# Kernel tuning notes

Hardware: AMD Instinct MI355X
Metric: run time of the kernel (lower is better)

The kernel has to match this reference:

```python
import jax, jax.numpy as jnp
import numpy as np

NEAR, FAR, N_SAMPLES = 1.0, 6.0, 64
FAR_APPEND = 1000.0


def setup_inputs() -> dict:
    key = jax.random.key(0)
    ks = jax.random.split(key, 8)
    B, R = 2, 4096
    # pixel coords in a 128x128 image
    x_pix = jax.random.uniform(ks[0], (B, R, 2), dtype=jnp.float32) * 128.0
    # plausible pinhole intrinsics (fx=fy=128, cx=cy=64)
    K = jnp.array([[128.0, 0.0, 64.0], [0.0, 128.0, 64.0], [0.0, 0.0, 1.0]], dtype=jnp.float32)
    intrinsics = jnp.tile(K[None], (B, 1, 1))
    # identity rotation, small translation cam2world
    c2w = jnp.eye(4, dtype=jnp.float32).at[:3, 3].set(jnp.array([0.1, -0.2, 0.5]))
    cam2world = jnp.tile(c2w[None], (B, 1, 1))
    H = 256
    W1 = jax.random.normal(ks[1], (3, H), dtype=jnp.float32) / np.sqrt(3.0)
    b1 = jnp.zeros((H,), jnp.float32)
    W2 = jax.random.normal(ks[2], (H, H), dtype=jnp.float32) / np.sqrt(H)
    b2 = jnp.zeros((H,), jnp.float32)
    W3 = jax.random.normal(ks[3], (H, 4), dtype=jnp.float32) / np.sqrt(H)
    b3 = jnp.zeros((4,), jnp.float32)
    return {"x_pix": x_pix, "intrinsics": intrinsics, "cam2world": cam2world,
            "W1": W1, "b1": b1, "W2": W2, "b2": b2, "W3": W3, "b3": b3}


def _radiance_field(pts, W1, b1, W2, b2, W3, b3):
    # pts: (B, N, 3) -> sigma (B, N, 1), rad (B, N, 3)
    h = jax.nn.relu(pts @ W1 + b1)
    h = jax.nn.relu(h @ W2 + b2)
    o = h @ W3 + b3
    return jax.nn.relu(o[..., :1]), jax.nn.sigmoid(o[..., 1:])


def _get_world_rays(x_pix, intrinsics, cam2world):
    B, R, _ = x_pix.shape
    inv_K = jnp.linalg.inv(intrinsics)  # (B,3,3)
    xy_hom = jnp.concatenate([x_pix, jnp.ones((B, R, 1), x_pix.dtype)], axis=-1)  # (B,R,3)
    dirs_cam = jnp.einsum("bij,brj->bri", inv_K, xy_hom)  # unnormalized cam-frame dirs
    dirs_hom = jnp.concatenate([dirs_cam, jnp.zeros((B, R, 1), x_pix.dtype)], axis=-1)  # w=0 vector
    dirs_world = jnp.einsum("bij,brj->bri", cam2world, dirs_hom)[..., :3]
    origins = jnp.broadcast_to(cam2world[:, None, :3, 3], (B, R, 3))
    return origins, dirs_world


def _volume_integral(z_vals, sigmas, radiances):
    # z_vals: (S,); sigmas: (B,R,S,1); radiances: (B,R,S,3)
    dists = jnp.diff(z_vals, append=jnp.array([FAR_APPEND], z_vals.dtype))  # (S,)
    alpha = 1.0 - jnp.exp(-sigmas * dists[None, None, :, None])  # (B,R,S,1)
    Ts = jnp.cumprod(1.0 - alpha, axis=2)  # inclusive cumprod, matching torch
    weights = alpha * Ts  # (B,R,S,1)
    rgb = jnp.sum(weights * radiances, axis=2)  # (B,R,3)
    depth_map = jnp.einsum("brsv,s->brv", weights, z_vals)  # (B,R,1)
    return rgb, depth_map, weights


def reference(x_pix, intrinsics, cam2world, W1, b1, W2, b2, W3, b3):
    B, R = x_pix.shape[0], x_pix.shape[1]
    ros, rds = _get_world_rays(x_pix, intrinsics, cam2world)
    z_vals = jnp.linspace(NEAR, FAR, N_SAMPLES, dtype=x_pix.dtype)  # (S,)
    pts = ros[:, :, None, :] + rds[:, :, None, :] * z_vals[None, None, :, None]  # (B,R,S,3)
    pts = pts.reshape(B, -1, 3)
    sigma, rad = _radiance_field(pts, W1, b1, W2, b2, W3, b3)
    sigma = sigma.reshape(B, R, N_SAMPLES, 1)
    rad = rad.reshape(B, R, N_SAMPLES, 3)
    rgb, depth_map, weights = _volume_integral(z_vals, sigma, rad)
    accum = jnp.sum(weights, axis=-2)  # (B,R,1)
    rgb = rgb + (1.0 - accum)  # white background
    return rgb, depth_map
```

## Files before the change

### kernel.cpp

```cpp
#include <hip/hip_runtime.h>

typedef unsigned short u16;
typedef _Float16 f16x8 __attribute__((ext_vector_type(8)));
typedef _Float16 f16x4 __attribute__((ext_vector_type(4)));
typedef float    f32x4 __attribute__((ext_vector_type(4)));

#define NRAYS 8192

#define WS_W2T  0
#define WS_B2   131072
#define WS_W3PT 132096
#define WS_B3   136192
#define WS_W1   136208
#define WS_B1   139280
#define WS_INTR 140304
#define WS_C2W  140384

__device__ __forceinline__ float bf2f(u16 u){
  union { unsigned int i; float f; } v; v.i = ((unsigned int)u) << 16; return v.f;
}
__device__ __forceinline__ u16 f2h(float f){
  union { _Float16 h; u16 u; } v; v.h = (_Float16)f;
  return v.u;
}
__device__ __forceinline__ int detect_bf16(const void* intr){
  return (((const u16*)intr)[0] == 0x4300u) ? 1 : 0;
}

__device__ __forceinline__ void conv_arr(const void* src, float* dst, int n, int bf, int tid){
  if (bf){
    const u16* s = (const u16*)src;
    for (int i = tid; i < n; i += 256) dst[i] = bf2f(s[i]);
  } else {
    const float* s = (const float*)src;
    for (int i = tid; i < n; i += 256) dst[i] = s[i];
  }
}

__global__ void prep(const void* __restrict__ W2, const void* __restrict__ W1,
                     const void* __restrict__ b1, const void* __restrict__ b2,
                     const void* __restrict__ W3, const void* __restrict__ b3,
                     const void* __restrict__ intr, const void* __restrict__ c2w,
                     char* __restrict__ ws)
{
  const int bf = detect_bf16(intr);
  const int t = threadIdx.x;
  if (blockIdx.x == 16){
    conv_arr(W1,  (float*)(ws + WS_W1),  768,  bf, t);
    conv_arr(b1,  (float*)(ws + WS_B1),  256,  bf, t);
    conv_arr(b2,  (float*)(ws + WS_B2),  256,  bf, t);
    conv_arr(b3,  (float*)(ws + WS_B3),  4,    bf, t);
    conv_arr(intr,(float*)(ws + WS_INTR),18,   bf, t);
    conv_arr(c2w, (float*)(ws + WS_C2W), 32,   bf, t);
    {
      u16* w3p = (u16*)(ws + WS_W3PT);
      for (int i = t; i < 1024; i += 256){
        int j = i >> 8, k = i & 255;
        float v = bf ? bf2f(((const u16*)W3)[k*4 + j]) : ((const float*)W3)[k*4 + j];
        w3p[i] = f2h(v);
      }
    }
    return;
  }
  __shared__ u16 tile[64][72];
  const int bx = blockIdx.x & 3;
  const int by = blockIdx.x >> 2;
  const int c = t & 63, rb = t >> 6;
  u16* W2T = (u16*)(ws + WS_W2T);
  #pragma unroll
  for (int rr = 0; rr < 64; rr += 4){
    int k = bx*64 + rr + rb;
    int n = by*64 + c;
    float v = bf ? bf2f(((const u16*)W2)[k*256 + n]) : ((const float*)W2)[k*256 + n];
    tile[rr + rb][c] = f2h(v);
  }
  __syncthreads();
  #pragma unroll
  for (int rr = 0; rr < 64; rr += 4){
    int n = by*64 + rr + rb;
    int k = bx*64 + c;
    W2T[n*256 + k] = tile[c][rr + rb];
  }
}

__global__ __launch_bounds__(256, 2) void nerf_fused(
    const void* __restrict__ x_pix,
    const void* __restrict__ intr,
    const char* __restrict__ ws,
    float* __restrict__ out)
{
  __shared__ __align__(16) u16 h1s[128 * 256];
  __shared__ __align__(16) float obuf[128 * 4];

  const int tid = threadIdx.x;
  const int l   = tid & 63;
  const int w   = tid >> 6;
  const int ray = w >> 1;
  const int rayg = blockIdx.x * 2 + ray;
  const int bb   = rayg >> 12;
  const int bf   = detect_bf16(intr);

  const float* intrf = (const float*)(ws + WS_INTR);
  const float* c2wf  = (const float*)(ws + WS_C2W);
  const float* W1f   = (const float*)(ws + WS_W1);
  const float* b1f   = (const float*)(ws + WS_B1);
  const float* b2f   = (const float*)(ws + WS_B2);
  const u16*   W3pT  = (const u16*)(ws + WS_W3PT);
  const u16*   W2T   = (const u16*)(ws + WS_W2T);

  float px, py;
  if (bf){
    px = bf2f(((const u16*)x_pix)[rayg*2 + 0]);
    py = bf2f(((const u16*)x_pix)[rayg*2 + 1]);
  } else {
    px = ((const float*)x_pix)[rayg*2 + 0];
    py = ((const float*)x_pix)[rayg*2 + 1];
  }
  float Ka[9], Mm[16];
  #pragma unroll
  for (int i = 0; i < 9;  i++) Ka[i] = intrf[bb*9  + i];
  #pragma unroll
  for (int i = 0; i < 16; i++) Mm[i] = c2wf[bb*16 + i];
  float a = Ka[0], b_ = Ka[1], c = Ka[2];
  float d = Ka[3], e  = Ka[4], f = Ka[5];
  float g = Ka[6], h  = Ka[7], i9 = Ka[8];
  float det = a*(e*i9 - f*h) - b_*(d*i9 - f*g) + c*(d*h - e*g);
  float inv = 1.0f / det;
  float i00 = (e*i9 - f*h)*inv, i01 = (c*h - b_*i9)*inv, i02 = (b_*f - c*e)*inv;
  float i10 = (f*g - d*i9)*inv, i11 = (a*i9 - c*g)*inv, i12 = (c*d - a*f)*inv;
  float i20 = (d*h - e*g)*inv,  i21 = (b_*g - a*h)*inv, i22 = (a*e - b_*d)*inv;
  float dcx = i00*px + i01*py + i02;
  float dcy = i10*px + i11*py + i12;
  float dcz = i20*px + i21*py + i22;
  float dx = Mm[0]*dcx + Mm[1]*dcy + Mm[2]*dcz;
  float dy = Mm[4]*dcx + Mm[5]*dcy + Mm[6]*dcz;
  float dz = Mm[8]*dcx + Mm[9]*dcy + Mm[10]*dcz;
  float ox = Mm[3], oy = Mm[7], oz = Mm[11];

  const int kbase = (w & 1)*128 + l*2;
  float aa0, aa1, gg0, gg1;
  {
    float2 r0 = *(const float2*)(W1f + kbase);
    float2 r1 = *(const float2*)(W1f + 256 + kbase);
    float2 r2 = *(const float2*)(W1f + 512 + kbase);
    float2 rb = *(const float2*)(b1f + kbase);
    aa0 = ox*r0.x + oy*r1.x + oz*r2.x + rb.x;
    aa1 = ox*r0.y + oy*r1.y + oz*r2.y + rb.y;
    gg0 = dx*r0.x + dy*r1.x + dz*r2.x;
    gg1 = dx*r0.y + dy*r1.y + dz*r2.y;
  }
  const float step = 5.0f / 63.0f;
  const int chunk_w = ((w & 1) << 4) + (l >> 2);
  const int sub_b   = (l & 3) << 2;
  {
    char* hb = (char*)h1s + (ray*64)*512;
    #pragma unroll 8
    for (int s = 0; s < 64; s++){
      float z = 1.0f + step * (float)s;
      u16 e0 = f2h(fmaxf(fmaf(gg0, z, aa0), 0.0f));
      u16 e1 = f2h(fmaxf(fmaf(gg1, z, aa1), 0.0f));
      unsigned pk = (unsigned)e0 | ((unsigned)e1 << 16);
      *(unsigned*)(hb + s*512 + ((chunk_w ^ (s & 7)) << 4) + sub_b) = pk;
    }
  }
  __syncthreads();

  const int col = l & 15;
  const int q   = l >> 4;
  const int c7  = col & 7;
  const int nbase = w * 64;

  f32x4 acc[4][8];
  #pragma unroll
  for (int nt = 0; nt < 4; nt++)
    #pragma unroll
    for (int mt = 0; mt < 8; mt++)
      acc[nt][mt] = (f32x4){0.f, 0.f, 0.f, 0.f};

  const u16* Ab = W2T + (nbase + col)*256 + q*8;
  const char* hbase = (const char*)h1s;

  f16x8 afc[4], bfc[8];
  #pragma unroll
  for (int nt = 0; nt < 4; nt++)
    afc[nt] = *(const f16x8*)(Ab + nt*16*256);
  {
    const int swz = (q ^ c7) << 4;
    #pragma unroll
    for (int mt = 0; mt < 8; mt++)
      bfc[mt] = *(const f16x8*)(hbase + (mt*16 + col)*512 + swz);
  }

  #pragma unroll
  for (int kc = 0; kc < 8; kc++){
    f16x8 afn[4], bfn[8];
    if (kc < 7){
      #pragma unroll
      for (int nt = 0; nt < 4; nt++)
        afn[nt] = *(const f16x8*)(Ab + nt*16*256 + (kc+1)*32);
      const int swz = (((kc+1)*4 + q) ^ c7) << 4;
      #pragma unroll
      for (int mt = 0; mt < 8; mt++)
        bfn[mt] = *(const f16x8*)(hbase + (mt*16 + col)*512 + swz);
    }
    #pragma unroll
    for (int nt = 0; nt < 4; nt++)
      #pragma unroll
      for (int mt = 0; mt < 8; mt++)
        acc[nt][mt] = __builtin_amdgcn_mfma_f32_16x16x32_f16(
            afc[nt], bfc[mt], acc[nt][mt], 0, 0, 0);
    if (kc < 7){
      #pragma unroll
      for (int nt = 0; nt < 4; nt++) afc[nt] = afn[nt];
      #pragma unroll
      for (int mt = 0; mt < 8; mt++) bfc[mt] = bfn[mt];
    }
  }

  f16x8 w3frag[8];
  {
    const u16* wp = W3pT + (col & 3)*256 + q*8;
    #pragma unroll
    for (int kc = 0; kc < 8; kc++)
      w3frag[kc] = *(const f16x8*)(wp + kc*32);
  }

  __syncthreads();
  #pragma unroll
  for (int nt = 0; nt < 4; nt++){
    const int n2 = nbase + nt*16 + q*4;
    const int chb = n2 >> 3;
    const int sub = (n2 & 7) * 2;
    f32x4 b2v = *(const f32x4*)(b2f + n2);
    #pragma unroll
    for (int mt = 0; mt < 8; mt++){
      const int m = mt*16 + col;
      f32x4 t = acc[nt][mt] + b2v;
      f16x4 hq;
      hq.x = (_Float16)fmaxf(t.x, 0.0f);
      hq.y = (_Float16)fmaxf(t.y, 0.0f);
      hq.z = (_Float16)fmaxf(t.z, 0.0f);
      hq.w = (_Float16)fmaxf(t.w, 0.0f);
      *(f16x4*)((char*)h1s + m*512 + ((chb ^ (m & 7)) << 4) + sub) = hq;
    }
  }
  __syncthreads();

  f32x4 acc3[2];
  acc3[0] = (f32x4){0.f,0.f,0.f,0.f};
  acc3[1] = (f32x4){0.f,0.f,0.f,0.f};
  #pragma unroll
  for (int mt3 = 0; mt3 < 2; mt3++){
    const int mrow = w*32 + mt3*16 + col;
    const int m7 = mrow & 7;
    #pragma unroll
    for (int kc = 0; kc < 8; kc++){
      f16x8 a3 = *(const f16x8*)((const char*)h1s + mrow*512 + (((kc*4 + q) ^ m7) << 4));
      acc3[mt3] = __builtin_amdgcn_mfma_f32_16x16x32_f16(a3, w3frag[kc], acc3[mt3], 0, 0, 0);
    }
  }
  if (col < 4){
    #pragma unroll
    for (int mt3 = 0; mt3 < 2; mt3++)
      #pragma unroll
      for (int rr = 0; rr < 4; rr++)
        obuf[(w*32 + mt3*16 + q*4 + rr)*4 + col] = acc3[mt3][rr];
  }
  __syncthreads();

  if (w < 2){
    const int m = w*64 + l;
    f32x4 oj  = *(const f32x4*)&obuf[m*4];
    f32x4 b3v = *(const f32x4*)(ws + WS_B3);
    float o_s0 = oj.x + b3v.x;
    float o_s1 = oj.y + b3v.y;
    float o_s2 = oj.z + b3v.z;
    float o_s3 = oj.w + b3v.w;

    const float zc    = 1.0f + step * (float)l;
    const float znext = (l == 63) ? 1000.0f : (1.0f + step * (float)(l + 1));
    const float dist  = znext - zc;
    float sigma = fmaxf(o_s0, 0.0f);
    float alpha = 1.0f - __expf(-sigma * dist);
    float t = 1.0f - alpha;
    #pragma unroll
    for (int sh = 1; sh < 64; sh <<= 1){
      float u = __shfl_up(t, sh, 64);
      if (l >= sh) t *= u;
    }
    float wgt = alpha * t;
    float r0 = 1.0f / (1.0f + __expf(-o_s1));
    float r1 = 1.0f / (1.0f + __expf(-o_s2));
    float r2 = 1.0f / (1.0f + __expf(-o_s3));
    float s0 = wgt*r0, s1 = wgt*r1, s2 = wgt*r2, sw = wgt, sz = wgt*zc;
    #pragma unroll
    for (int sh = 1; sh < 64; sh <<= 1){
      s0 += __shfl_xor(s0, sh, 64);
      s1 += __shfl_xor(s1, sh, 64);
      s2 += __shfl_xor(s2, sh, 64);
      sw += __shfl_xor(sw, sh, 64);
      sz += __shfl_xor(sz, sh, 64);
    }
    if (l == 0){
      const int rg = blockIdx.x*2 + w;
      float bg = 1.0f - sw;
      out[rg*3 + 0] = s0 + bg;
      out[rg*3 + 1] = s1 + bg;
      out[rg*3 + 2] = s2 + bg;
      out[3*NRAYS + rg] = sz;
    }
  }
}

extern "C" void kernel_launch(void* const* d_in, const int* in_sizes, int n_in,
                              void* d_out, int out_size, void* d_ws, size_t ws_size,
                              hipStream_t stream)
{
  const void* x_pix = d_in[0];
  const void* intr  = d_in[1];
  const void* c2w   = d_in[2];
  const void* W1    = d_in[3];
  const void* b1    = d_in[4];
  const void* W2    = d_in[5];
  const void* b2    = d_in[6];
  const void* W3    = d_in[7];
  const void* b3    = d_in[8];
  float* outp = (float*)d_out;
  char*  ws   = (char*)d_ws;

  hipLaunchKernelGGL(prep, dim3(17), dim3(256), 0, stream,
                     W2, W1, b1, b2, W3, b3, intr, c2w, ws);
  hipLaunchKernelGGL(nerf_fused, dim3(NRAYS/2), dim3(256), 0, stream,
                     x_pix, intr, ws, outp);
}
```

Before: 183.1 us.

## Use 512-thread blocks with 8 waves splitting GEMM N dimension

Doubles the block size to 512 threads (8 waves), so each wave computes a 32-column slice of the 256x256 layer-2 GEMM instead of 64, halving accumulator registers. Layer-1 generation now writes one fp16 element per thread, and the B-fragment loads are restructured into two half-batches per k-chunk rather than fully double-buffered. The aim is lower VGPR pressure and more resident waves to hide latency. In exchange there is less register prefetching, more LDS B-fragment reads per MFMA across waves, and narrower 16-bit LDS stores.

```diff
diff --git a/kernel.cpp b/kernel.cpp
--- a/kernel.cpp
+++ b/kernel.cpp
@@ -83,7 +83,7 @@
   }
 }
 
-__global__ __launch_bounds__(256, 2) void nerf_fused(
+__global__ __launch_bounds__(512, 4) void nerf_fused(
     const void* __restrict__ x_pix,
     const void* __restrict__ intr,
     const char* __restrict__ ws,
@@ -95,7 +95,7 @@
   const int tid = threadIdx.x;
   const int l   = tid & 63;
   const int w   = tid >> 6;
-  const int ray = w >> 1;
+  const int ray = w >> 2;
   const int rayg = blockIdx.x * 2 + ray;
   const int bb   = rayg >> 12;
   const int bf   = detect_bf16(intr);
@@ -137,30 +137,23 @@
   float dz = Mm[8]*dcx + Mm[9]*dcy + Mm[10]*dcz;
   float ox = Mm[3], oy = Mm[7], oz = Mm[11];
 
-  const int kbase = (w & 1)*128 + l*2;
-  float aa0, aa1, gg0, gg1;
+  const int kk = (w & 3)*64 + l;
+  float aa, gg;
   {
-    float2 r0 = *(const float2*)(W1f + kbase);
-    float2 r1 = *(const float2*)(W1f + 256 + kbase);
-    float2 r2 = *(const float2*)(W1f + 512 + kbase);
-    float2 rb = *(const float2*)(b1f + kbase);
-    aa0 = ox*r0.x + oy*r1.x + oz*r2.x + rb.x;
-    aa1 = ox*r0.y + oy*r1.y + oz*r2.y + rb.y;
-    gg0 = dx*r0.x + dy*r1.x + dz*r2.x;
-    gg1 = dx*r0.y + dy*r1.y + dz*r2.y;
+    float r0 = W1f[kk], r1 = W1f[256 + kk], r2 = W1f[512 + kk], rb = b1f[kk];
+    aa = ox*r0 + oy*r1 + oz*r2 + rb;
+    gg = dx*r0 + dy*r1 + dz*r2;
   }
   const float step = 5.0f / 63.0f;
-  const int chunk_w = ((w & 1) << 4) + (l >> 2);
-  const int sub_b   = (l & 3) << 2;
   {
+    const int chunk = kk >> 3;
+    const int sub_b = (kk & 7) * 2;
     char* hb = (char*)h1s + (ray*64)*512;
     #pragma unroll 8
     for (int s = 0; s < 64; s++){
       float z = 1.0f + step * (float)s;
-      u16 e0 = f2h(fmaxf(fmaf(gg0, z, aa0), 0.0f));
-      u16 e1 = f2h(fmaxf(fmaf(gg1, z, aa1), 0.0f));
-      unsigned pk = (unsigned)e0 | ((unsigned)e1 << 16);
-      *(unsigned*)(hb + s*512 + ((chunk_w ^ (s & 7)) << 4) + sub_b) = pk;
+      u16 e0 = f2h(fmaxf(fmaf(gg, z, aa), 0.0f));
+      *(u16*)(hb + s*512 + ((chunk ^ (s & 7)) << 4) + sub_b) = e0;
     }
   }
   __syncthreads();
@@ -168,11 +161,11 @@
   const int col = l & 15;
   const int q   = l >> 4;
   const int c7  = col & 7;
-  const int nbase = w * 64;
-
-  f32x4 acc[4][8];
-  #pragma unroll
-  for (int nt = 0; nt < 4; nt++)
+  const int nbase = w * 32;
+
+  f32x4 acc[2][8];
+  #pragma unroll
+  for (int nt = 0; nt < 2; nt++)
     #pragma unroll
     for (int mt = 0; mt < 8; mt++)
       acc[nt][mt] = (f32x4){0.f, 0.f, 0.f, 0.f};
@@ -180,56 +173,39 @@
   const u16* Ab = W2T + (nbase + col)*256 + q*8;
   const char* hbase = (const char*)h1s;
 
-  f16x8 afc[4], bfc[8];
-  #pragma unroll
-  for (int nt = 0; nt < 4; nt++)
-    afc[nt] = *(const f16x8*)(Ab + nt*16*256);
-  {
-    const int swz = (q ^ c7) << 4;
-    #pragma unroll
-    for (int mt = 0; mt < 8; mt++)
-      bfc[mt] = *(const f16x8*)(hbase + (mt*16 + col)*512 + swz);
-  }
+  f16x8 afc[2];
+  afc[0] = *(const f16x8*)(Ab);
+  afc[1] = *(const f16x8*)(Ab + 16*256);
 
   #pragma unroll
   for (int kc = 0; kc < 8; kc++){
-    f16x8 afn[4], bfn[8];
+    f16x8 afn[2];
     if (kc < 7){
+      afn[0] = *(const f16x8*)(Ab + (kc+1)*32);
+      afn[1] = *(const f16x8*)(Ab + 16*256 + (kc+1)*32);
+    }
+    const int swz = ((kc*4 + q) ^ c7) << 4;
+    #pragma unroll
+    for (int mh = 0; mh < 2; mh++){
+      f16x8 bfr[4];
       #pragma unroll
-      for (int nt = 0; nt < 4; nt++)
-        afn[nt] = *(const f16x8*)(Ab + nt*16*256 + (kc+1)*32);
-      const int swz = (((kc+1)*4 + q) ^ c7) << 4;
+      for (int m4 = 0; m4 < 4; m4++)
+        bfr[m4] = *(const f16x8*)(hbase + ((mh*4 + m4)*16 + col)*512 + swz);
       #pragma unroll
-      for (int mt = 0; mt < 8; mt++)
-        bfn[mt] = *(const f16x8*)(hbase + (mt*16 + col)*512 + swz);
-    }
-    #pragma unroll
-    for (int nt = 0; nt < 4; nt++)
-      #pragma unroll
-      for (int mt = 0; mt < 8; mt++)
-        acc[nt][mt] = __builtin_amdgcn_mfma_f32_16x16x32_f16(
-            afc[nt], bfc[mt], acc[nt][mt], 0, 0, 0);
-    if (kc < 7){
-      #pragma unroll
-      for (int nt = 0; nt < 4; nt++) afc[nt] = afn[nt];
-      #pragma unroll
-      for (int mt = 0; mt < 8; mt++) bfc[mt] = bfn[mt];
-    }
-  }
-
-  f16x8 w3frag[8];
-  {
-    const u16* wp = W3pT + (col & 3)*256 + q*8;
-    #pragma unroll
-    for (int kc = 0; kc < 8; kc++)
-      w3frag[kc] = *(const f16x8*)(wp + kc*32);
-  }
-
-  __syncthreads();
-  #pragma unroll
-  for (int nt = 0; nt < 4; nt++){
+      for (int nt = 0; nt < 2; nt++)
+        #pragma unroll
+        for (int m4 = 0; m4 < 4; m4++)
+          acc[nt][mh*4 + m4] = __builtin_amdgcn_mfma_f32_16x16x32_f16(
+              afc[nt], bfr[m4], acc[nt][mh*4 + m4], 0, 0, 0);
+    }
+    if (kc < 7){ afc[0] = afn[0]; afc[1] = afn[1]; }
+  }
+
+  __syncthreads();
+  #pragma unroll
+  for (int nt = 0; nt < 2; nt++){
     const int n2 = nbase + nt*16 + q*4;
-    const int chb = n2 >> 3;
+    const int xo = ((n2 >> 3) ^ c7) << 4;
     const int sub = (n2 & 7) * 2;
     f32x4 b2v = *(const f32x4*)(b2f + n2);
     #pragma unroll
@@ -241,30 +217,32 @@
       hq.y = (_Float16)fmaxf(t.y, 0.0f);
       hq.z = (_Float16)fmaxf(t.z, 0.0f);
       hq.w = (_Float16)fmaxf(t.w, 0.0f);
-      *(f16x4*)((char*)h1s + m*512 + ((chb ^ (m & 7)) << 4) + sub) = hq;
-    }
-  }
-  __syncthreads();
-
-  f32x4 acc3[2];
-  acc3[0] = (f32x4){0.f,0.f,0.f,0.f};
-  acc3[1] = (f32x4){0.f,0.f,0.f,0.f};
-  #pragma unroll
-  for (int mt3 = 0; mt3 < 2; mt3++){
-    const int mrow = w*32 + mt3*16 + col;
-    const int m7 = mrow & 7;
+      *(f16x4*)((char*)h1s + m*512 + xo + sub) = hq;
+    }
+  }
+  __syncthreads();
+
+  f16x8 w3frag[8];
+  {
+    const u16* wp = W3pT + (col & 3)*256 + q*8;
+    #pragma unroll
+    for (int kc = 0; kc < 8; kc++)
+      w3frag[kc] = *(const f16x8*)(wp + kc*32);
+  }
+  f32x4 acc3 = (f32x4){0.f,0.f,0.f,0.f};
+  {
+    const int mrow = w*16 + col;
+    const int m7 = col & 7;
     #pragma unroll
     for (int kc = 0; kc < 8; kc++){
       f16x8 a3 = *(const f16x8*)((const char*)h1s + mrow*512 + (((kc*4 + q) ^ m7) << 4));
-      acc3[mt3] = __builtin_amdgcn_mfma_f32_16x16x32_f16(a3, w3frag[kc], acc3[mt3], 0, 0, 0);
+      acc3 = __builtin_amdgcn_mfma_f32_16x16x32_f16(a3, w3frag[kc], acc3, 0, 0, 0);
     }
   }
   if (col < 4){
     #pragma unroll
-    for (int mt3 = 0; mt3 < 2; mt3++)
-      #pragma unroll
-      for (int rr = 0; rr < 4; rr++)
-        obuf[(w*32 + mt3*16 + q*4 + rr)*4 + col] = acc3[mt3][rr];
+    for (int rr = 0; rr < 4; rr++)
+      obuf[(w*16 + q*4 + rr)*4 + col] = acc3[rr];
   }
   __syncthreads();
 
@@ -330,6 +308,6 @@
 
   hipLaunchKernelGGL(prep, dim3(17), dim3(256), 0, stream,
                      W2, W1, b1, b2, W3, b3, intr, c2w, ws);
-  hipLaunchKernelGGL(nerf_fused, dim3(NRAYS/2), dim3(256), 0, stream,
+  hipLaunchKernelGGL(nerf_fused, dim3(NRAYS/2), dim3(512), 0, stream,
                      x_pix, intr, ws, outp);
 }
```

Result: slower. 192.3 us (+5.0%).
